# Kernel tuning notes

Hardware: AMD Instinct MI355X
Metric: run time of the kernel (lower is better)

Reference implementation:

```python
import jax, jax.numpy as jnp
import numpy as np

MIN_DECAY = 0.8
N_SAMPLES = 32768
N_FRAMES = 128
D = 128
BATCH = 128
N_EVENTS = 8
START = 8      # ConvUpsample start size
SLOPE = 0.2    # leaky_relu negative slope


def _tconv(x, w, b):
    # ConvTranspose1d(kernel=4, stride=2, padding=1) -> doubles length.
    # Equivalent dilated conv needs explicit padding k-1-p = 2 per side.
    y = jax.lax.conv_transpose(x, w, strides=(2,), padding=[(2, 2)],
                               dimension_numbers=('NCH', 'IOH', 'NCH'))
    return y + b[None, :, None]


def setup_inputs() -> dict:
    key = jax.random.key(0)
    ks = jax.random.split(key, 16)
    s = 0.1  # weight_init
    inp = {
        'x': jax.random.normal(ks[0], (BATCH, N_EVENTS, D), jnp.float32),
        'noise': jax.random.uniform(ks[1], (BATCH * N_EVENTS, 1, N_SAMPLES), jnp.float32, -10.0, 10.0),
        'Wup': jax.random.normal(ks[2], (D, D * START), jnp.float32) * s,
        'bup': jnp.zeros((D * START,), jnp.float32),
    }
    for i in range(3):
        inp[f'Wd{i}'] = jax.random.normal(ks[3 + i], (D, D), jnp.float32) * s
        inp[f'bd{i}'] = jnp.zeros((D,), jnp.float32)
    inp['Wdo'] = jax.random.normal(ks[6], (D, 1), jnp.float32) * s
    inp['bdo'] = jnp.zeros((1,), jnp.float32)
    chans = [D, D, D, D, 1]  # frames: 8->16->32->64->128, last layer to 1 channel
    for i in range(4):
        inp[f'Wc{i}'] = jax.random.normal(ks[7 + i], (chans[i], chans[i + 1], 4), jnp.float32) * s
        inp[f'bc{i}'] = jnp.zeros((chans[i + 1],), jnp.float32)
    return inp


def reference(x, noise, Wup, bup, Wd0, bd0, Wd1, bd1, Wd2, bd2, Wdo, bdo,
              Wc0, bc0, Wc1, bc1, Wc2, bc2, Wc3, bc3):
    B, E, Dm = x.shape
    xf = x.reshape(-1, Dm)                      # [BE, D]
    # decay head: LinearOutputStack(D, 3, out_channels=1)
    h = xf
    for W, b in ((Wd0, bd0), (Wd1, bd1), (Wd2, bd2)):
        h = jax.nn.leaky_relu(h @ W + b, SLOPE)
    decay = MIN_DECAY + jax.nn.sigmoid(h @ Wdo + bdo) * (1.0 - MIN_DECAY)  # [BE, 1]
    # ConvUpsample('learned'): linear -> [BE, D, 8] -> 4 doubling tconvs -> [BE, 1, F]
    u = (xf @ Wup + bup).reshape(-1, Dm, START)
    u = jax.nn.leaky_relu(_tconv(u, Wc0, bc0), SLOPE)
    u = jax.nn.leaky_relu(_tconv(u, Wc1, bc1), SLOPE)
    u = jax.nn.leaky_relu(_tconv(u, Wc2, bc2), SLOPE)
    u = _tconv(u, Wc3, bc3)                     # [BE, 1, F]
    u = u ** 2
    # exponential-decay recurrence: v[i] = u[i] + decay * v[i-1]
    def step(carry, ut):
        v = ut + decay * carry
        return v, v
    seq = jnp.moveaxis(u, -1, 0)                # [F, BE, 1]
    _, vs = jax.lax.scan(step, jnp.zeros_like(seq[0]), seq)
    v = jnp.moveaxis(vs, 0, -1)                 # [BE, 1, F]
    # linear interpolation F -> N_SAMPLES (align_corners=False)
    pos = (jnp.arange(N_SAMPLES) + 0.5) * (N_FRAMES / N_SAMPLES) - 0.5
    pos = jnp.clip(pos, 0.0, N_FRAMES - 1)
    i0 = jnp.floor(pos).astype(jnp.int32)
    i1 = jnp.minimum(i0 + 1, N_FRAMES - 1)
    w = (pos - i0).astype(v.dtype)
    out = v[..., i0] * (1.0 - w) + v[..., i1] * w  # [BE, 1, N]
    out = out * noise
    return out.reshape(B, E, 1, N_SAMPLES)
```

## Files before the change

kernel.cpp:

```cpp
#include <hip/hip_runtime.h>

#define SLOPE 0.2f
__device__ __forceinline__ float lrelu(float v){ return v > 0.0f ? v : SLOPE*v; }

template<int L, bool RELU>
__device__ __forceinline__ void tconv_q(const float* __restrict__ W,
                                        const float* __restrict__ bias,
                                        const float* __restrict__ in,
                                        float* __restrict__ out,
                                        int co, int q)
{
  constexpr int TQ = L/2;
  constexpr int NI = L/4;
  const int i0 = q*NI;
  float acc[TQ];
  {
    const float b = bias[co];
    #pragma unroll
    for (int j=0;j<TQ;j++) acc[j]=b;
  }
  const bool hasM1 = (q > 0);
  const bool hasE  = (q < 3);
  #pragma unroll 2
  for (int ci=0; ci<128; ci++){
    const float4 w = *(const float4*)(W + ((size_t)ci*128 + co)*4);
    const float* xin = in + ci*L + i0;
    const float xm1 = hasM1 ? xin[-1] : 0.0f;
    const float xE  = hasE  ? xin[NI] : 0.0f;
    float xv[NI];
    if constexpr (NI==2){ const float2 t=*(const float2*)xin; xv[0]=t.x; xv[1]=t.y; }
    else if constexpr (NI==4){ const float4 t=*(const float4*)xin;
      xv[0]=t.x; xv[1]=t.y; xv[2]=t.z; xv[3]=t.w; }
    else {
      const float4 t0=*(const float4*)xin; const float4 t1=*(const float4*)(xin+4);
      xv[0]=t0.x; xv[1]=t0.y; xv[2]=t0.z; xv[3]=t0.w;
      xv[4]=t1.x; xv[5]=t1.y; xv[6]=t1.z; xv[7]=t1.w;
    }
    acc[0]    += xm1*w.x;
    acc[TQ-1] += xE *w.w;
    #pragma unroll
    for (int li=0; li<NI; li++){
      const float x = xv[li];
      acc[2*li]   += x*w.z;
      acc[2*li+1] += x*w.y;
      if (li<NI-1) acc[2*li+2] += x*w.x;
      if (li>0)    acc[2*li-1] += x*w.w;
    }
  }
  float* op = out + co*(2*L) + q*TQ;
  #pragma unroll
  for (int j=0;j<TQ;j++) op[j] = RELU ? lrelu(acc[j]) : acc[j];
}

extern "C" __global__ __launch_bounds__(512, 6)
void npg_compute(const float* __restrict__ x,
                 const float* __restrict__ noise,
                 const float* __restrict__ Wup, const float* __restrict__ bup,
                 const float* __restrict__ Wd0, const float* __restrict__ bd0,
                 const float* __restrict__ Wd1, const float* __restrict__ bd1,
                 const float* __restrict__ Wd2, const float* __restrict__ bd2,
                 const float* __restrict__ Wdo, const float* __restrict__ bdo,
                 const float* __restrict__ Wc0, const float* __restrict__ bc0,
                 const float* __restrict__ Wc1, const float* __restrict__ bc1,
                 const float* __restrict__ Wc2, const float* __restrict__ bc2,
                 const float* __restrict__ Wc3, const float* __restrict__ bc3,
                 float* __restrict__ outp)
{
  __shared__ float bufB[128*64];
  __shared__ float bufA[128*32];
  __shared__ float part[512];
  __shared__ float sdecay;

  float* const xrow = bufB;
  float* const h0   = bufB + 128;
  float* const h1   = bufB + 256;
  float* const fr   = bufA;

  const int tid = threadIdx.x;
  const int row = blockIdx.x;
  const int c   = tid & 127;
  const int g   = tid >> 7;

  if (tid < 128) xrow[tid] = x[row*128 + tid];
  __syncthreads();

  {
    const float* inb = xrow;
    const float* Ws[3] = {Wd0, Wd1, Wd2};
    const float* bs[3] = {bd0, bd1, bd2};
    float* outs[3] = {h0, h1, h0};
    #pragma unroll
    for (int layer=0; layer<3; layer++){
      float a = 0.0f;
      const int base = g*32;
      const float* W = Ws[layer];
      #pragma unroll 8
      for (int i=0;i<32;i++) a += inb[base+i]*W[(size_t)(base+i)*128 + c];
      part[g*128 + c] = a;
      __syncthreads();
      if (tid < 128){
        const float v = part[tid]+part[128+tid]+part[256+tid]+part[384+tid] + bs[layer][tid];
        outs[layer][tid] = lrelu(v);
      }
      __syncthreads();
      inb = outs[layer];
    }
    if (tid < 128) part[tid] = h0[tid]*Wdo[tid];
    __syncthreads();
    if (tid < 64){
      float v = part[tid] + part[tid+64];
      #pragma unroll
      for (int off=32; off>0; off>>=1) v += __shfl_down(v, off, 64);
      if (tid==0){
        const float z = v + bdo[0];
        sdecay = 0.8f + 0.2f/(1.0f + expf(-z));
      }
    }
    __syncthreads();
  }

  {
    const int o = tid*2;
    float2 a = make_float2(bup[o], bup[o+1]);
    #pragma unroll 4
    for (int i=0;i<128;i++){
      const float xv = xrow[i];
      const float2 w = *(const float2*)(Wup + (size_t)i*1024 + o);
      a.x += xv*w.x; a.y += xv*w.y;
    }
    bufA[o] = a.x; bufA[o+1] = a.y;
    __syncthreads();
  }

  tconv_q<8 , true>(Wc0, bc0, bufA, bufB, c, g); __syncthreads();
  tconv_q<16, true>(Wc1, bc1, bufB, bufA, c, g); __syncthreads();
  tconv_q<32, true>(Wc2, bc2, bufA, bufB, c, g); __syncthreads();

  {
    const int t = c;
    const bool even = ((t & 1) == 0);
    const int i  = t >> 1;
    const int ia = even ? (i-1) : i;
    const int ib = even ? i : (i+1);
    const float ma = (ia >= 0) ? 1.0f : 0.0f;
    const float mb = (ib < 64) ? 1.0f : 0.0f;
    const int iac = (ia >= 0) ? ia : 0;
    const int ibc = (ib < 64) ? ib : 63;
    float a = 0.0f;
    const int cb = g*32;
    #pragma unroll 4
    for (int k=0;k<32;k++){
      const int ci = cb + k;
      const float4 w = *(const float4*)(Wc3 + (size_t)ci*4);
      const float wa = even ? w.x : w.y;
      const float wb = even ? w.z : w.w;
      a += (bufB[ci*64 + iac]*ma)*wa + (bufB[ci*64 + ibc]*mb)*wb;
    }
    part[g*128 + t] = a;
    __syncthreads();
    if (tid < 128){
      const float s = part[tid]+part[128+tid]+part[256+tid]+part[384+tid] + bc3[0];
      fr[tid] = s*s;
    }
    __syncthreads();
  }

  {
    float d = sdecay;
    #pragma unroll
    for (int o=1;o<128;o<<=1){
      const float prev = (tid < 128 && tid >= o) ? fr[tid-o] : 0.0f;
      __syncthreads();
      if (tid < 128) fr[tid] += d*prev;
      __syncthreads();
      d = d*d;
    }
  }

  {
    const float4* __restrict__ nz4 = (const float4*)(noise + (size_t)row*32768);
    float4*       __restrict__ o4  = (float4*)(outp  + (size_t)row*32768);
    #pragma unroll 8
    for (int it=0; it<16; ++it){
      const int idx = it*512 + tid;
      const float4 nz = nz4[idx];
      const int n = idx*4;
      float r[4];
      #pragma unroll
      for (int j=0;j<4;j++){
        float pos = ((float)(n+j) + 0.5f) * (1.0f/256.0f) - 0.5f;
        pos = fminf(fmaxf(pos, 0.0f), 127.0f);
        const int i0 = (int)pos;
        const int i1 = min(i0+1, 127);
        const float w = pos - (float)i0;
        r[j] = fr[i0]*(1.0f-w) + fr[i1]*w;
      }
      float4 o;
      o.x = r[0]*nz.x; o.y = r[1]*nz.y; o.z = r[2]*nz.z; o.w = r[3]*nz.w;
      o4[idx] = o;
    }
  }
}

extern "C" void kernel_launch(void* const* d_in, const int* in_sizes, int n_in,
                              void* d_out, int out_size, void* d_ws, size_t ws_size,
                              hipStream_t stream)
{
  const float* x    = (const float*)d_in[0];
  const float* noise= (const float*)d_in[1];
  const float* Wup  = (const float*)d_in[2];
  const float* bup  = (const float*)d_in[3];
  const float* Wd0  = (const float*)d_in[4];
  const float* bd0  = (const float*)d_in[5];
  const float* Wd1  = (const float*)d_in[6];
  const float* bd1  = (const float*)d_in[7];
  const float* Wd2  = (const float*)d_in[8];
  const float* bd2  = (const float*)d_in[9];
  const float* Wdo  = (const float*)d_in[10];
  const float* bdo  = (const float*)d_in[11];
  const float* Wc0  = (const float*)d_in[12];
  const float* bc0  = (const float*)d_in[13];
  const float* Wc1  = (const float*)d_in[14];
  const float* bc1  = (const float*)d_in[15];
  const float* Wc2  = (const float*)d_in[16];
  const float* bc2  = (const float*)d_in[17];
  const float* Wc3  = (const float*)d_in[18];
  const float* bc3  = (const float*)d_in[19];
  float* out = (float*)d_out;

  hipLaunchKernelGGL(npg_compute, dim3(1024), dim3(512), 0, stream,
                     x, noise, Wup, bup, Wd0, bd0, Wd1, bd1, Wd2, bd2, Wdo, bdo,
                     Wc0, bc0, Wc1, bc1, Wc2, bc2, Wc3, bc3, out);
}
```

Before: 482.0 us.

## Tile last tconv stages in halves to shrink LDS and raise occupancy

```diff
diff --git a/kernel.cpp b/kernel.cpp
--- a/kernel.cpp
+++ b/kernel.cpp
@@ -3,39 +3,36 @@
 #define SLOPE 0.2f
 __device__ __forceinline__ float lrelu(float v){ return v > 0.0f ? v : SLOPE*v; }
 
-template<int L, bool RELU>
-__device__ __forceinline__ void tconv_q(const float* __restrict__ W,
-                                        const float* __restrict__ bias,
-                                        const float* __restrict__ in,
-                                        float* __restrict__ out,
-                                        int co, int q)
-{
-  constexpr int TQ = L/2;
-  constexpr int NI = L/4;
-  const int i0 = q*NI;
+template<int LT, int LF, int IS, int OS, bool RELU>
+__device__ __forceinline__ void tconv_tile(const float* __restrict__ W,
+                                           const float* __restrict__ bias,
+                                           const float* __restrict__ in,
+                                           int base,
+                                           float* __restrict__ out,
+                                           int obase,
+                                           int co, int q)
+{
+  constexpr int TQ = LT/2;
+  constexpr int NI = LT/4;
+  const int i0 = base + q*NI;
   float acc[TQ];
   {
     const float b = bias[co];
     #pragma unroll
     for (int j=0;j<TQ;j++) acc[j]=b;
   }
-  const bool hasM1 = (q > 0);
-  const bool hasE  = (q < 3);
+  const bool hasM1 = (i0 > 0);
+  const bool hasE  = (i0 + NI < LF);
   #pragma unroll 2
   for (int ci=0; ci<128; ci++){
     const float4 w = *(const float4*)(W + ((size_t)ci*128 + co)*4);
-    const float* xin = in + ci*L + i0;
+    const float* xin = in + ci*IS + i0;
     const float xm1 = hasM1 ? xin[-1] : 0.0f;
     const float xE  = hasE  ? xin[NI] : 0.0f;
     float xv[NI];
     if constexpr (NI==2){ const float2 t=*(const float2*)xin; xv[0]=t.x; xv[1]=t.y; }
-    else if constexpr (NI==4){ const float4 t=*(const float4*)xin;
+    else { const float4 t=*(const float4*)xin;
       xv[0]=t.x; xv[1]=t.y; xv[2]=t.z; xv[3]=t.w; }
-    else {
-      const float4 t0=*(const float4*)xin; const float4 t1=*(const float4*)(xin+4);
-      xv[0]=t0.x; xv[1]=t0.y; xv[2]=t0.z; xv[3]=t0.w;
-      xv[4]=t1.x; xv[5]=t1.y; xv[6]=t1.z; xv[7]=t1.w;
-    }
     acc[0]    += xm1*w.x;
     acc[TQ-1] += xE *w.w;
     #pragma unroll
@@ -47,12 +44,50 @@
       if (li>0)    acc[2*li-1] += x*w.w;
     }
   }
-  float* op = out + co*(2*L) + q*TQ;
+  float* op = out + co*OS + obase + q*TQ;
   #pragma unroll
   for (int j=0;j<TQ;j++) op[j] = RELU ? lrelu(acc[j]) : acc[j];
 }
 
-extern "C" __global__ __launch_bounds__(512, 6)
+__device__ __forceinline__ void final_tile(const float* __restrict__ Wc3,
+                                           const float* __restrict__ bc3,
+                                           const float* __restrict__ bufC,
+                                           float* __restrict__ part,
+                                           float* __restrict__ fr,
+                                           int tt, int c, int g, int tid)
+{
+  const int off = tt*32;
+  const int t = c;
+  const bool inwin = (tt==0) ? (t < 63) : (t >= 63);
+  const bool even = ((t & 1) == 0);
+  const int i  = t >> 1;
+  const int ia = even ? (i-1) : i;
+  const int ib = even ? i : (i+1);
+  const int sa = ia - off + 1;
+  const int sbr = ib - off + 1;
+  const float mb = (sbr <= 32) ? 1.0f : 0.0f;
+  const int sb = (sbr <= 32) ? sbr : 32;
+  float a = 0.0f;
+  if (inwin){
+    const int cb = g*32;
+    #pragma unroll 4
+    for (int k=0;k<32;k++){
+      const int ci = cb + k;
+      const float4 w = *(const float4*)(Wc3 + (size_t)ci*4);
+      const float wa = even ? w.x : w.y;
+      const float wb = even ? w.z : w.w;
+      a += bufC[ci*33 + sa]*wa + (bufC[ci*33 + sb]*mb)*wb;
+    }
+  }
+  part[g*128 + t] = a;
+  __syncthreads();
+  if (tid < 128 && ((tt==0) ? (tid < 63) : (tid >= 63))){
+    const float s = part[tid]+part[128+tid]+part[256+tid]+part[384+tid] + bc3[0];
+    fr[tid] = s*s;
+  }
+}
+
+extern "C" __global__ __launch_bounds__(512, 8)
 void npg_compute(const float* __restrict__ x,
                  const float* __restrict__ noise,
                  const float* __restrict__ Wup, const float* __restrict__ bup,
@@ -66,15 +101,15 @@
                  const float* __restrict__ Wc3, const float* __restrict__ bc3,
                  float* __restrict__ outp)
 {
-  __shared__ float bufB[128*64];
-  __shared__ float bufA[128*32];
+  __shared__ float R0[128*32];
+  __shared__ float R1[128*33];
   __shared__ float part[512];
+  __shared__ float fr[128];
   __shared__ float sdecay;
 
-  float* const xrow = bufB;
-  float* const h0   = bufB + 128;
-  float* const h1   = bufB + 256;
-  float* const fr   = bufA;
+  float* const xrow = R1;
+  float* const h0   = R1 + 128;
+  float* const h1   = R1 + 256;
 
   const int tid = threadIdx.x;
   const int row = blockIdx.x;
@@ -128,42 +163,29 @@
       const float2 w = *(const float2*)(Wup + (size_t)i*1024 + o);
       a.x += xv*w.x; a.y += xv*w.y;
     }
-    bufA[o] = a.x; bufA[o+1] = a.y;
+    R0[o] = a.x; R0[o+1] = a.y;
     __syncthreads();
   }
 
-  tconv_q<8 , true>(Wc0, bc0, bufA, bufB, c, g); __syncthreads();
-  tconv_q<16, true>(Wc1, bc1, bufB, bufA, c, g); __syncthreads();
-  tconv_q<32, true>(Wc2, bc2, bufA, bufB, c, g); __syncthreads();
-
-  {
-    const int t = c;
-    const bool even = ((t & 1) == 0);
-    const int i  = t >> 1;
-    const int ia = even ? (i-1) : i;
-    const int ib = even ? i : (i+1);
-    const float ma = (ia >= 0) ? 1.0f : 0.0f;
-    const float mb = (ib < 64) ? 1.0f : 0.0f;
-    const int iac = (ia >= 0) ? ia : 0;
-    const int ibc = (ib < 64) ? ib : 63;
-    float a = 0.0f;
-    const int cb = g*32;
-    #pragma unroll 4
-    for (int k=0;k<32;k++){
-      const int ci = cb + k;
-      const float4 w = *(const float4*)(Wc3 + (size_t)ci*4);
-      const float wa = even ? w.x : w.y;
-      const float wb = even ? w.z : w.w;
-      a += (bufB[ci*64 + iac]*ma)*wa + (bufB[ci*64 + ibc]*mb)*wb;
-    }
-    part[g*128 + t] = a;
-    __syncthreads();
-    if (tid < 128){
-      const float s = part[tid]+part[128+tid]+part[256+tid]+part[384+tid] + bc3[0];
-      fr[tid] = s*s;
-    }
-    __syncthreads();
-  }
+  tconv_tile<8 , 8, 8, 16, true>(Wc0, bc0, R0, 0, R1, 0, c, g);  __syncthreads();
+  tconv_tile<16,16,16, 32, true>(Wc1, bc1, R1, 0, R0, 0, c, g);  __syncthreads();
+
+  tconv_tile<16,32,32, 33, true>(Wc2, bc2, R0, 0, R1, 1, c, g);
+  if (tid < 128) R1[tid*33] = 0.0f;
+  __syncthreads();
+
+  final_tile(Wc3, bc3, R1, part, fr, 0, c, g, tid);
+  if (tid >= 128 && tid < 256){
+    const int ci = tid - 128;
+    R1[ci*33] = R1[ci*33 + 32];
+  }
+  __syncthreads();
+
+  tconv_tile<16,32,32, 33, true>(Wc2, bc2, R0, 16, R1, 1, c, g);
+  __syncthreads();
+
+  final_tile(Wc3, bc3, R1, part, fr, 1, c, g, tid);
+  __syncthreads();
 
   {
     float d = sdecay;
```

After: 465.1 us. 3.5% less time.
